# Performance work log

Hardware: AMD Instinct MI355X
Metric: run time of the kernel (lower is better)

The kernel has to match this reference:

```python
import jax, jax.numpy as jnp
import numpy as np

N = 100000
K = 16
C_IN = 64
C_MID = 64   # max(in_channels, out_channels // 2)
C_OUT = 128
EPS = 1e-5


def setup_inputs() -> dict:
    key = jax.random.key(0)
    ks = jax.random.split(key, 4)
    feat = jax.random.normal(ks[0], (N, C_IN), dtype=jnp.float32)
    reference_index = jax.random.randint(ks[1], (N, K), 0, N, dtype=jnp.int64)
    # Kaiming-ish init for the two Linear layers (torch Linear default scale)
    W1 = jax.random.normal(ks[2], (C_IN, C_MID), dtype=jnp.float32) / np.sqrt(C_IN)
    W2 = jax.random.normal(ks[3], (C_MID, C_OUT), dtype=jnp.float32) / np.sqrt(C_MID)
    return {
        "feat": feat,
        "reference_index": reference_index,
        "W1": W1,
        "b1": jnp.zeros((C_MID,), jnp.float32),
        "gamma1": jnp.ones((C_MID,), jnp.float32),
        "beta1": jnp.zeros((C_MID,), jnp.float32),
        "W2": W2,
        "b2": jnp.zeros((C_OUT,), jnp.float32),
        "gamma2": jnp.ones((C_OUT,), jnp.float32),
        "beta2": jnp.zeros((C_OUT,), jnp.float32),
    }


def _bn(x, gamma, beta):
    # BatchNorm1d in training mode: biased batch stats over the row dim.
    mean = jnp.mean(x, axis=0)
    var = jnp.var(x, axis=0)
    return (x - mean) * jax.lax.rsqrt(var + EPS) * gamma + beta


def reference(feat, reference_index, W1, b1, gamma1, beta1, W2, b2, gamma2, beta2):
    # grouping (with_xyz=False): gather neighbor features -> [N, K, C_IN]
    grouped = feat[reference_index]
    x = grouped.reshape(-1, C_IN)                 # [N*K, C_IN]
    h = jax.nn.relu(_bn(x @ W1 + b1, gamma1, beta1))   # [N*K, C_MID]
    h = jax.nn.relu(_bn(h @ W2 + b2, gamma2, beta2))   # [N*K, C_OUT]
    out = h.reshape(N, K, C_OUT).max(axis=1)      # max-pool over neighbors
    return out
```

## Files before the change

kernel.cpp:

```cpp
#include <hip/hip_runtime.h>
#include <hip/hip_bf16.h>

#define N_PTS 100000
#define KNN   16
#define NK    (N_PTS * KNN)
#define CIN   64
#define CMID  64
#define COUT  128

#define HSLC    64
#define SEG_CNT 25000
#define SEG_U32 12500

#define NCOPY 32

#define OFF_PC    0
#define OFF_HB    0
#define OFF_SP1   13000000
#define OFF_SP2   13100000
#define OFF_Z1B   25600000
#define OFF_CNT   38400000
#define OFF_W2BF  38801536
#define OFF_W1BF  38817920

typedef __attribute__((ext_vector_type(8))) short bf16x8;
typedef __attribute__((ext_vector_type(4))) float f32x4;
union U8 { uint4 u; bf16x8 v; unsigned short s[8]; };

__device__ __forceinline__ unsigned short f2bf(float f) {
    unsigned u = __float_as_uint(f);
    unsigned r = (u + 0x7fffu + ((u >> 16) & 1u)) >> 16;
    return (unsigned short)r;
}

__global__ __launch_bounds__(256) void hist_k(const int* __restrict__ idx,
                                              unsigned short* __restrict__ pc,
                                              const float* __restrict__ W2,
                                              unsigned short* __restrict__ w2bf,
                                              const float* __restrict__ W1,
                                              unsigned short* __restrict__ w1bf,
                                              float* __restrict__ sp1,
                                              float* __restrict__ sp2) {
    if (blockIdx.x >= 256) {
        if (blockIdx.x == 256) {
            for (int e = threadIdx.x; e < 8192; e += 256) {
                int j = e & 7, lane = (e >> 3) & 63, kh = (e >> 9) & 1, nt = e >> 10;
                int k = kh * 32 + (lane >> 4) * 8 + j;
                int n = nt * 16 + (lane & 15);
                w2bf[e] = f2bf(W2[k * COUT + n]);
            }
        } else if (blockIdx.x == 257) {
            for (int e = threadIdx.x; e < 4096; e += 256) {
                int j = e & 7, lane = (e >> 3) & 63, kh = (e >> 9) & 1, nt = e >> 10;
                int k = kh * 32 + (lane >> 4) * 8 + j;
                int n = nt * 16 + (lane & 15);
                w1bf[e] = f2bf(W1[k * CMID + n]);
            }
        } else {
            for (int i = threadIdx.x; i < NCOPY * 128; i += 256) sp1[i] = 0.f;
            for (int i = threadIdx.x; i < NCOPY * 256; i += 256) sp2[i] = 0.f;
        }
        return;
    }
    __shared__ unsigned int smem[SEG_U32];
    int seg  = blockIdx.x & 3;
    int slc  = blockIdx.x >> 2;
    int base = seg * SEG_CNT;

    for (int i = threadIdx.x; i < SEG_U32; i += 256) smem[i] = 0;
    __syncthreads();

    const int4* ip = (const int4*)idx;
    const int per = NK / 4 / HSLC;
    int s = slc * per, e = s + per;
    for (int i = s + threadIdx.x; i < e; i += 256) {
        int4 v = ip[i];
        int a;
        a = v.x - base; if ((unsigned)a < (unsigned)SEG_CNT)
            atomicAdd(&smem[a >> 1], 1u << ((a & 1) * 16));
        a = v.y - base; if ((unsigned)a < (unsigned)SEG_CNT)
            atomicAdd(&smem[a >> 1], 1u << ((a & 1) * 16));
        a = v.z - base; if ((unsigned)a < (unsigned)SEG_CNT)
            atomicAdd(&smem[a >> 1], 1u << ((a & 1) * 16));
        a = v.w - base; if ((unsigned)a < (unsigned)SEG_CNT)
            atomicAdd(&smem[a >> 1], 1u << ((a & 1) * 16));
    }
    __syncthreads();

    unsigned int* outp = (unsigned int*)(pc + (size_t)slc * N_PTS) + seg * SEG_U32;
    for (int i = threadIdx.x; i < SEG_U32; i += 256) outp[i] = smem[i];
}

__global__ __launch_bounds__(256) void gemm1_k(const float* __restrict__ feat,
                                               const unsigned short* __restrict__ w1bf,
                                               const float* __restrict__ b1,
                                               const unsigned short* __restrict__ pc,
                                               float* __restrict__ counts,
                                               unsigned short* __restrict__ z1b,
                                               float* __restrict__ sp1) {
    int lane = threadIdx.x & 63, wid = threadIdx.x >> 6;
    int il = lane & 15, quad = lane >> 4;

    bf16x8 wf[4][2];
    const uint4* wp = (const uint4*)w1bf;
    #pragma unroll
    for (int nt = 0; nt < 4; nt++) {
        U8 t0; t0.u = wp[(nt * 2 + 0) * 64 + lane]; wf[nt][0] = t0.v;
        U8 t1; t1.u = wp[(nt * 2 + 1) * 64 + lane]; wf[nt][1] = t1.v;
    }
    float bias[4];
    #pragma unroll
    for (int nt = 0; nt < 4; nt++) bias[nt] = b1[nt * 16 + il];

    float s[4] = {0, 0, 0, 0}, q[4] = {0, 0, 0, 0};

    int wgid = blockIdx.x * 4 + wid;
    for (int tile = wgid; tile < N_PTS / 16; tile += gridDim.x * 4) {
        int m0 = tile * 16;

        const uint4* pcp = (const uint4*)(pc + (size_t)lane * N_PTS + m0);
        uint4 pa = pcp[0], pb = pcp[1];
        #pragma unroll
        for (int m = 1; m < 64; m <<= 1) {
            pa.x += __shfl_xor(pa.x, m, 64);
            pa.y += __shfl_xor(pa.y, m, 64);
            pa.z += __shfl_xor(pa.z, m, 64);
            pa.w += __shfl_xor(pa.w, m, 64);
            pb.x += __shfl_xor(pb.x, m, 64);
            pb.y += __shfl_xor(pb.y, m, 64);
            pb.z += __shfl_xor(pb.z, m, 64);
            pb.w += __shfl_xor(pb.w, m, 64);
        }
        unsigned w0 = (quad == 0) ? pa.x : (quad == 1) ? pa.z : (quad == 2) ? pb.x : pb.z;
        unsigned w1 = (quad == 0) ? pa.y : (quad == 1) ? pa.w : (quad == 2) ? pb.y : pb.w;
        float4 cnt4;
        cnt4.x = (float)(w0 & 0xffffu);
        cnt4.y = (float)(w0 >> 16);
        cnt4.z = (float)(w1 & 0xffffu);
        cnt4.w = (float)(w1 >> 16);
        if (il == 0) ((float4*)(counts + m0))[quad] = cnt4;

        const float* fr = feat + (size_t)(m0 + il) * 64;
        float4 fa = *(const float4*)(fr + quad * 8);
        float4 fb = *(const float4*)(fr + quad * 8 + 4);
        float4 fc = *(const float4*)(fr + 32 + quad * 8);
        float4 fd = *(const float4*)(fr + 32 + quad * 8 + 4);
        U8 ua, ub;
        ua.s[0] = f2bf(fa.x); ua.s[1] = f2bf(fa.y); ua.s[2] = f2bf(fa.z); ua.s[3] = f2bf(fa.w);
        ua.s[4] = f2bf(fb.x); ua.s[5] = f2bf(fb.y); ua.s[6] = f2bf(fb.z); ua.s[7] = f2bf(fb.w);
        ub.s[0] = f2bf(fc.x); ub.s[1] = f2bf(fc.y); ub.s[2] = f2bf(fc.z); ub.s[3] = f2bf(fc.w);
        ub.s[4] = f2bf(fd.x); ub.s[5] = f2bf(fd.y); ub.s[6] = f2bf(fd.z); ub.s[7] = f2bf(fd.w);

        #pragma unroll
        for (int nt = 0; nt < 4; nt++) {
            f32x4 acc = {bias[nt], bias[nt], bias[nt], bias[nt]};
            acc = __builtin_amdgcn_mfma_f32_16x16x32_bf16(ua.v, wf[nt][0], acc, 0, 0, 0);
            acc = __builtin_amdgcn_mfma_f32_16x16x32_bf16(ub.v, wf[nt][1], acc, 0, 0, 0);
            unsigned short* zp = z1b + (size_t)(m0 + quad * 4) * 64 + nt * 16 + il;
            zp[0]   = f2bf(acc[0]);
            zp[64]  = f2bf(acc[1]);
            zp[128] = f2bf(acc[2]);
            zp[192] = f2bf(acc[3]);
            s[nt] += cnt4.x * acc[0] + cnt4.y * acc[1] + cnt4.z * acc[2] + cnt4.w * acc[3];
            q[nt] += cnt4.x * acc[0] * acc[0] + cnt4.y * acc[1] * acc[1]
                   + cnt4.z * acc[2] * acc[2] + cnt4.w * acc[3] * acc[3];
        }
    }
    #pragma unroll
    for (int m = 16; m <= 32; m <<= 1) {
        #pragma unroll
        for (int nt = 0; nt < 4; nt++) {
            s[nt] += __shfl_xor(s[nt], m, 64);
            q[nt] += __shfl_xor(q[nt], m, 64);
        }
    }
    __shared__ float sred[2][4][4][16];
    if (quad == 0) {
        #pragma unroll
        for (int nt = 0; nt < 4; nt++) { sred[0][wid][nt][il] = s[nt]; sred[1][wid][nt][il] = q[nt]; }
    }
    __syncthreads();
    if (threadIdx.x < 128) {
        int which = threadIdx.x >> 6, c = threadIdx.x & 63;
        float t = sred[which][0][c >> 4][c & 15] + sred[which][1][c >> 4][c & 15]
                + sred[which][2][c >> 4][c & 15] + sred[which][3][c >> 4][c & 15];
        atomicAdd(&sp1[(blockIdx.x & (NCOPY - 1)) * 128 + threadIdx.x], t);
    }
}

__device__ __forceinline__ bf16x8 bnrelu(uint4 r, float4 alo, float4 ahi,
                                         float4 blo, float4 bhi) {
    float z0 = __uint_as_float(r.x << 16), z1 = __uint_as_float(r.x & 0xffff0000u);
    float z2 = __uint_as_float(r.y << 16), z3 = __uint_as_float(r.y & 0xffff0000u);
    float z4 = __uint_as_float(r.z << 16), z5 = __uint_as_float(r.z & 0xffff0000u);
    float z6 = __uint_as_float(r.w << 16), z7 = __uint_as_float(r.w & 0xffff0000u);
    U8 o;
    o.s[0] = f2bf(fmaxf(fmaf(alo.x, z0, blo.x), 0.f));
    o.s[1] = f2bf(fmaxf(fmaf(alo.y, z1, blo.y), 0.f));
    o.s[2] = f2bf(fmaxf(fmaf(alo.z, z2, blo.z), 0.f));
    o.s[3] = f2bf(fmaxf(fmaf(alo.w, z3, blo.w), 0.f));
    o.s[4] = f2bf(fmaxf(fmaf(ahi.x, z4, bhi.x), 0.f));
    o.s[5] = f2bf(fmaxf(fmaf(ahi.y, z5, bhi.y), 0.f));
    o.s[6] = f2bf(fmaxf(fmaf(ahi.z, z6, bhi.z), 0.f));
    o.s[7] = f2bf(fmaxf(fmaf(ahi.w, z7, bhi.w), 0.f));
    return o.v;
}

__global__ __launch_bounds__(256) void stats2_k(const unsigned short* __restrict__ z1b,
                                                const unsigned short* __restrict__ w2bf,
                                                const float* __restrict__ sp1,
                                                const float* __restrict__ g1,
                                                const float* __restrict__ be1,
                                                const float* __restrict__ b2,
                                                const float* __restrict__ counts,
                                                unsigned short* __restrict__ hb,
                                                float* __restrict__ sp2) {
    __shared__ float Sl[128];
    __shared__ float Al[64], Bl[64];
    if (threadIdx.x < 128) {
        float t = 0.f;
        #pragma unroll
        for (int k = 0; k < NCOPY; k++) t += sp1[k * 128 + threadIdx.x];
        Sl[threadIdx.x] = t;
    }
    __syncthreads();
    if (threadIdx.x < 64) {
        const float inv = 1.0f / (float)NK;
        float m = Sl[threadIdx.x] * inv;
        float v = Sl[64 + threadIdx.x] * inv - m * m;
        float a = g1[threadIdx.x] * rsqrtf(v + 1e-5f);
        Al[threadIdx.x] = a;
        Bl[threadIdx.x] = be1[threadIdx.x] - m * a;
    }
    __syncthreads();

    int lane = threadIdx.x & 63, wid = threadIdx.x >> 6;
    int il = lane & 15, quad = lane >> 4;

    float4 a0lo = *(const float4*)(Al + quad * 8);
    float4 a0hi = *(const float4*)(Al + quad * 8 + 4);
    float4 b0lo = *(const float4*)(Bl + quad * 8);
    float4 b0hi = *(const float4*)(Bl + quad * 8 + 4);
    float4 a1lo = *(const float4*)(Al + 32 + quad * 8);
    float4 a1hi = *(const float4*)(Al + 32 + quad * 8 + 4);
    float4 b1lo = *(const float4*)(Bl + 32 + quad * 8);
    float4 b1hi = *(const float4*)(Bl + 32 + quad * 8 + 4);

    bf16x8 bfr[8][2];
    const uint4* wp = (const uint4*)w2bf;
    #pragma unroll
    for (int nt = 0; nt < 8; nt++) {
        U8 t0; t0.u = wp[(nt * 2 + 0) * 64 + lane]; bfr[nt][0] = t0.v;
        U8 t1; t1.u = wp[(nt * 2 + 1) * 64 + lane]; bfr[nt][1] = t1.v;
    }
    float bias[8];
    #pragma unroll
    for (int nt = 0; nt < 8; nt++) bias[nt] = b2[nt * 16 + il];

    float s[8], q[8];
    #pragma unroll
    for (int j = 0; j < 8; j++) { s[j] = 0.f; q[j] = 0.f; }

    int wgid = blockIdx.x * 4 + wid;
    for (int tile = wgid; tile < N_PTS / 16; tile += gridDim.x * 4) {
        int m0 = tile * 16;
        const uint4* ar = (const uint4*)(z1b + (size_t)(m0 + il) * 64);
        uint4 ra0 = ar[quad];
        uint4 ra1 = ar[4 + quad];
        bf16x8 af0 = bnrelu(ra0, a0lo, a0hi, b0lo, b0hi);
        bf16x8 af1 = bnrelu(ra1, a1lo, a1hi, b1lo, b1hi);
        U8 o0; o0.v = af0;
        U8 o1; o1.v = af1;
        uint4* hp = (uint4*)(hb + (size_t)(m0 + il) * 64);
        hp[quad]     = o0.u;
        hp[4 + quad] = o1.u;
        float4 cnt4 = *(const float4*)(counts + m0 + quad * 4);
        #pragma unroll
        for (int nt = 0; nt < 8; nt++) {
            f32x4 acc = {bias[nt], bias[nt], bias[nt], bias[nt]};
            acc = __builtin_amdgcn_mfma_f32_16x16x32_bf16(af0, bfr[nt][0], acc, 0, 0, 0);
            acc = __builtin_amdgcn_mfma_f32_16x16x32_bf16(af1, bfr[nt][1], acc, 0, 0, 0);
            s[nt] += cnt4.x * acc[0] + cnt4.y * acc[1] + cnt4.z * acc[2] + cnt4.w * acc[3];
            q[nt] += cnt4.x * acc[0] * acc[0] + cnt4.y * acc[1] * acc[1]
                   + cnt4.z * acc[2] * acc[2] + cnt4.w * acc[3] * acc[3];
        }
    }
    #pragma unroll
    for (int m = 16; m <= 32; m <<= 1) {
        #pragma unroll
        for (int nt = 0; nt < 8; nt++) {
            s[nt] += __shfl_xor(s[nt], m, 64);
            q[nt] += __shfl_xor(q[nt], m, 64);
        }
    }
    __shared__ float sred[2][4][8][16];
    if (quad == 0) {
        #pragma unroll
        for (int nt = 0; nt < 8; nt++) { sred[0][wid][nt][il] = s[nt]; sred[1][wid][nt][il] = q[nt]; }
    }
    __syncthreads();
    {
        int which = threadIdx.x >> 7, c = threadIdx.x & 127;
        float t = sred[which][0][c >> 4][c & 15] + sred[which][1][c >> 4][c & 15]
                + sred[which][2][c >> 4][c & 15] + sred[which][3][c >> 4][c & 15];
        atomicAdd(&sp2[(blockIdx.x & (NCOPY - 1)) * 256 + threadIdx.x], t);
    }
}

__global__ __launch_bounds__(256) void fused_k(const unsigned short* __restrict__ hb,
                                               const unsigned short* __restrict__ w2bf,
                                               const int* __restrict__ idx,
                                               const float* __restrict__ b2,
                                               const float* __restrict__ sp2,
                                               const float* __restrict__ g2,
                                               const float* __restrict__ be2,
                                               float* __restrict__ out) {
    __shared__ float S2l[256];
    __shared__ float A2s[128], B2f[128];
    __shared__ uint4 wlds[1024];

    {
        float t = 0.f;
        #pragma unroll
        for (int k = 0; k < NCOPY; k++) t += sp2[k * 256 + threadIdx.x];
        S2l[threadIdx.x] = t;
    }
    __syncthreads();
    const float inv = 1.0f / (float)NK;
    if (threadIdx.x < 128) {
        int c = threadIdx.x;
        float m = S2l[c] * inv;
        float v = S2l[128 + c] * inv - m * m;
        float a = g2[c] * rsqrtf(v + 1e-5f);
        A2s[c] = a;
        B2f[c] = fmaf(a, b2[c], be2[c] - m * a);
    }
    __syncthreads();

    for (int i = threadIdx.x; i < 1024; i += 256) {
        uint4 w = ((const uint4*)w2bf)[i];
        int n_ = ((i >> 7) << 4) + (i & 15);
        if (A2s[n_] < 0.f) {
            w.x ^= 0x80008000u; w.y ^= 0x80008000u;
            w.z ^= 0x80008000u; w.w ^= 0x80008000u;
        }
        wlds[i] = w;
    }
    __syncthreads();

    int lane = threadIdx.x & 63, wid = threadIdx.x >> 6;
    int il = lane & 15, quad = lane >> 4;

    bf16x8 bfr[8][2];
    #pragma unroll
    for (int nt = 0; nt < 8; nt++) {
        U8 t0; t0.u = wlds[(nt * 2 + 0) * 64 + lane]; bfr[nt][0] = t0.v;
        U8 t1; t1.u = wlds[(nt * 2 + 1) * 64 + lane]; bfr[nt][1] = t1.v;
    }
    float a2c[8], b2c[8];
    #pragma unroll
    for (int nt = 0; nt < 8; nt++) {
        a2c[nt] = fabsf(A2s[nt * 16 + il]);
        b2c[nt] = B2f[nt * 16 + il];
    }

    const int stride = gridDim.x * 4;
    int n  = blockIdx.x * 4 + wid;
    int n1 = n + stride;

    uint4 r0c = {0, 0, 0, 0}, r1c = {0, 0, 0, 0};
    if (n < N_PTS) {
        int j0 = idx[(size_t)n * KNN + il];
        const uint4* zr = (const uint4*)(hb + (size_t)j0 * 64);
        r0c = zr[quad];
        r1c = zr[4 + quad];
    }
    int j1 = (n1 < N_PTS) ? idx[(size_t)n1 * KNN + il] : 0;

    while (n < N_PTS) {
        uint4 r0n = {0, 0, 0, 0}, r1n = {0, 0, 0, 0};
        int n2 = n1 + stride;
        if (n1 < N_PTS) {
            const uint4* zr = (const uint4*)(hb + (size_t)j1 * 64);
            r0n = zr[quad];
            r1n = zr[4 + quad];
        }
        int j2 = (n2 < N_PTS) ? idx[(size_t)n2 * KNN + il] : 0;

        U8 ua, ub; ua.u = r0c; ub.u = r1c;
        float w0 = 0.f, w1 = 0.f;
        #pragma unroll
        for (int nt = 0; nt < 8; nt++) {
            f32x4 acc = {0.f, 0.f, 0.f, 0.f};
            acc = __builtin_amdgcn_mfma_f32_16x16x32_bf16(ua.v, bfr[nt][0], acc, 0, 0, 0);
            acc = __builtin_amdgcn_mfma_f32_16x16x32_bf16(ub.v, bfr[nt][1], acc, 0, 0, 0);
            float t = fmaxf(fmaxf(acc[0], acc[1]), fmaxf(acc[2], acc[3]));
            t = fmaxf(t, __shfl_xor(t, 16, 64));
            t = fmaxf(t, __shfl_xor(t, 32, 64));
            float v = fmaxf(fmaf(a2c[nt], t, b2c[nt]), 0.f);
            if (nt == quad)     w0 = v;
            if (nt == quad + 4) w1 = v;
        }
        float* op = out + (size_t)n * COUT;
        __builtin_nontemporal_store(w0, op + quad * 16 + il);
        __builtin_nontemporal_store(w1, op + 64 + quad * 16 + il);

        n = n1; n1 = n2; j1 = j2;
        r0c = r0n; r1c = r1n;
    }
}

extern "C" void kernel_launch(void* const* d_in, const int* in_sizes, int n_in,
                              void* d_out, int out_size, void* d_ws, size_t ws_size,
                              hipStream_t stream) {
    const float* feat = (const float*)d_in[0];
    const int*   idx  = (const int*)d_in[1];
    const float* W1   = (const float*)d_in[2];
    const float* b1   = (const float*)d_in[3];
    const float* g1   = (const float*)d_in[4];
    const float* be1  = (const float*)d_in[5];
    const float* W2   = (const float*)d_in[6];
    const float* b2   = (const float*)d_in[7];
    const float* g2   = (const float*)d_in[8];
    const float* be2  = (const float*)d_in[9];
    float* out = (float*)d_out;

    char* ws = (char*)d_ws;
    unsigned short* pc  = (unsigned short*)(ws + OFF_PC);
    unsigned short* hb  = (unsigned short*)(ws + OFF_HB);
    float* sp1 = (float*)(ws + OFF_SP1);
    float* sp2 = (float*)(ws + OFF_SP2);
    unsigned short* z1b = (unsigned short*)(ws + OFF_Z1B);
    float* counts = (float*)(ws + OFF_CNT);
    unsigned short* w2bf = (unsigned short*)(ws + OFF_W2BF);
    unsigned short* w1bf = (unsigned short*)(ws + OFF_W1BF);

    hist_k<<<259, 256, 0, stream>>>(idx, pc, W2, w2bf, W1, w1bf, sp1, sp2);
    gemm1_k<<<512, 256, 0, stream>>>(feat, w1bf, b1, pc, counts, z1b, sp1);
    stats2_k<<<512, 256, 0, stream>>>(z1b, w2bf, sp1, g1, be1, b2, counts, hb, sp2);
    fused_k<<<2048, 256, 0, stream>>>(hb, w2bf, idx, b2, sp2, g2, be2, out);
}
```

Before: 180.0 us.

## Use 32x32x16 MFMA in fused kernel, processing two points per wave

The final fused gather-GEMM-maxpool kernel switches from 16x16x32 bf16 MFMA on one point per wave to 32x32x16 MFMA covering two points (32 neighbor rows) per wave. A second W2 bf16 layout matching the 32x32 operand format is built in the prep kernel. This halves the loop trip count, cuts the cross-lane shuffles needed for the max reduction, and makes each lane store one contiguous output value per column tile. In exchange it needs more accumulator registers and an extra weight layout in the workspace.

```diff
diff --git a/kernel.cpp b/kernel.cpp
--- a/kernel.cpp
+++ b/kernel.cpp
@@ -14,17 +14,19 @@
 
 #define NCOPY 32
 
-#define OFF_PC    0
-#define OFF_HB    0
-#define OFF_SP1   13000000
-#define OFF_SP2   13100000
-#define OFF_Z1B   25600000
-#define OFF_CNT   38400000
-#define OFF_W2BF  38801536
-#define OFF_W1BF  38817920
+#define OFF_PC     0
+#define OFF_HB     0
+#define OFF_SP1    13000000
+#define OFF_SP2    13100000
+#define OFF_W2BF32 13200000
+#define OFF_Z1B    25600000
+#define OFF_CNT    38400000
+#define OFF_W2BF   38801536
+#define OFF_W1BF   38817920
 
 typedef __attribute__((ext_vector_type(8))) short bf16x8;
 typedef __attribute__((ext_vector_type(4))) float f32x4;
+typedef __attribute__((ext_vector_type(16))) float f32x16;
 union U8 { uint4 u; bf16x8 v; unsigned short s[8]; };
 
 __device__ __forceinline__ unsigned short f2bf(float f) {
@@ -37,6 +39,7 @@
                                               unsigned short* __restrict__ pc,
                                               const float* __restrict__ W2,
                                               unsigned short* __restrict__ w2bf,
+                                              unsigned short* __restrict__ w2bf32,
                                               const float* __restrict__ W1,
                                               unsigned short* __restrict__ w1bf,
                                               float* __restrict__ sp1,
@@ -48,6 +51,13 @@
                 int k = kh * 32 + (lane >> 4) * 8 + j;
                 int n = nt * 16 + (lane & 15);
                 w2bf[e] = f2bf(W2[k * COUT + n]);
+            }
+            for (int e = threadIdx.x; e < 8192; e += 256) {
+                int j = e & 7, lane = (e >> 3) & 63, f = e >> 9;
+                int kc = f & 3, nt2 = f >> 2;
+                int k = kc * 16 + (lane >> 5) * 8 + j;
+                int n = nt2 * 32 + (lane & 31);
+                w2bf32[e] = f2bf(W2[k * COUT + n]);
             }
         } else if (blockIdx.x == 257) {
             for (int e = threadIdx.x; e < 4096; e += 256) {
@@ -308,7 +318,7 @@
 }
 
 __global__ __launch_bounds__(256) void fused_k(const unsigned short* __restrict__ hb,
-                                               const unsigned short* __restrict__ w2bf,
+                                               const unsigned short* __restrict__ w2bf32,
                                                const int* __restrict__ idx,
                                                const float* __restrict__ b2,
                                                const float* __restrict__ sp2,
@@ -338,9 +348,9 @@
     __syncthreads();
 
     for (int i = threadIdx.x; i < 1024; i += 256) {
-        uint4 w = ((const uint4*)w2bf)[i];
-        int n_ = ((i >> 7) << 4) + (i & 15);
-        if (A2s[n_] < 0.f) {
+        uint4 w = ((const uint4*)w2bf32)[i];
+        int c = ((i >> 8) << 5) + (i & 31);
+        if (A2s[c] < 0.f) {
             w.x ^= 0x80008000u; w.y ^= 0x80008000u;
             w.z ^= 0x80008000u; w.w ^= 0x80008000u;
         }
@@ -349,64 +359,73 @@
     __syncthreads();
 
     int lane = threadIdx.x & 63, wid = threadIdx.x >> 6;
-    int il = lane & 15, quad = lane >> 4;
-
-    bf16x8 bfr[8][2];
-    #pragma unroll
-    for (int nt = 0; nt < 8; nt++) {
-        U8 t0; t0.u = wlds[(nt * 2 + 0) * 64 + lane]; bfr[nt][0] = t0.v;
-        U8 t1; t1.u = wlds[(nt * 2 + 1) * 64 + lane]; bfr[nt][1] = t1.v;
-    }
-    float a2c[8], b2c[8];
-    #pragma unroll
-    for (int nt = 0; nt < 8; nt++) {
-        a2c[nt] = fabsf(A2s[nt * 16 + il]);
-        b2c[nt] = B2f[nt * 16 + il];
-    }
-
+    int r32 = lane & 31;
+    int hi  = lane >> 5;
+    int pl  = (lane >> 4) & 1;
+    int nb  = lane & 15;
+
+    bf16x8 bfr[4][4];
+    #pragma unroll
+    for (int nt2 = 0; nt2 < 4; nt2++) {
+        #pragma unroll
+        for (int kc = 0; kc < 4; kc++) {
+            U8 t; t.u = wlds[(nt2 * 4 + kc) * 64 + lane];
+            bfr[nt2][kc] = t.v;
+        }
+    }
+    float a2c[4], b2c[4];
+    #pragma unroll
+    for (int nt2 = 0; nt2 < 4; nt2++) {
+        a2c[nt2] = fabsf(A2s[nt2 * 32 + r32]);
+        b2c[nt2] = B2f[nt2 * 32 + r32];
+    }
+
+    const int NPAIRS = N_PTS / 2;
     const int stride = gridDim.x * 4;
-    int n  = blockIdx.x * 4 + wid;
-    int n1 = n + stride;
-
-    uint4 r0c = {0, 0, 0, 0}, r1c = {0, 0, 0, 0};
-    if (n < N_PTS) {
-        int j0 = idx[(size_t)n * KNN + il];
-        const uint4* zr = (const uint4*)(hb + (size_t)j0 * 64);
-        r0c = zr[quad];
-        r1c = zr[4 + quad];
-    }
-    int j1 = (n1 < N_PTS) ? idx[(size_t)n1 * KNN + il] : 0;
-
-    while (n < N_PTS) {
-        uint4 r0n = {0, 0, 0, 0}, r1n = {0, 0, 0, 0};
-        int n2 = n1 + stride;
-        if (n1 < N_PTS) {
-            const uint4* zr = (const uint4*)(hb + (size_t)j1 * 64);
-            r0n = zr[quad];
-            r1n = zr[4 + quad];
-        }
-        int j2 = (n2 < N_PTS) ? idx[(size_t)n2 * KNN + il] : 0;
-
-        U8 ua, ub; ua.u = r0c; ub.u = r1c;
-        float w0 = 0.f, w1 = 0.f;
-        #pragma unroll
-        for (int nt = 0; nt < 8; nt++) {
-            f32x4 acc = {0.f, 0.f, 0.f, 0.f};
-            acc = __builtin_amdgcn_mfma_f32_16x16x32_bf16(ua.v, bfr[nt][0], acc, 0, 0, 0);
-            acc = __builtin_amdgcn_mfma_f32_16x16x32_bf16(ub.v, bfr[nt][1], acc, 0, 0, 0);
-            float t = fmaxf(fmaxf(acc[0], acc[1]), fmaxf(acc[2], acc[3]));
-            t = fmaxf(t, __shfl_xor(t, 16, 64));
-            t = fmaxf(t, __shfl_xor(t, 32, 64));
-            float v = fmaxf(fmaf(a2c[nt], t, b2c[nt]), 0.f);
-            if (nt == quad)     w0 = v;
-            if (nt == quad + 4) w1 = v;
-        }
-        float* op = out + (size_t)n * COUT;
-        __builtin_nontemporal_store(w0, op + quad * 16 + il);
-        __builtin_nontemporal_store(w1, op + 64 + quad * 16 + il);
-
-        n = n1; n1 = n2; j1 = j2;
-        r0c = r0n; r1c = r1n;
+    int pair = blockIdx.x * 4 + wid;
+    int p1 = pair + stride;
+
+    uint4 rc0 = {0,0,0,0}, rc1 = {0,0,0,0}, rc2 = {0,0,0,0}, rc3 = {0,0,0,0};
+    if (pair < NPAIRS) {
+        int j0 = idx[(size_t)(pair * 2 + pl) * KNN + nb];
+        const uint4* zr = (const uint4*)hb + (size_t)j0 * 8;
+        rc0 = zr[0 + hi]; rc1 = zr[2 + hi]; rc2 = zr[4 + hi]; rc3 = zr[6 + hi];
+    }
+    int j1 = (p1 < NPAIRS) ? idx[(size_t)(p1 * 2 + pl) * KNN + nb] : 0;
+
+    while (pair < NPAIRS) {
+        uint4 rn0 = {0,0,0,0}, rn1 = {0,0,0,0}, rn2 = {0,0,0,0}, rn3 = {0,0,0,0};
+        int p2 = p1 + stride;
+        if (p1 < NPAIRS) {
+            const uint4* zr = (const uint4*)hb + (size_t)j1 * 8;
+            rn0 = zr[0 + hi]; rn1 = zr[2 + hi]; rn2 = zr[4 + hi]; rn3 = zr[6 + hi];
+        }
+        int j2 = (p2 < NPAIRS) ? idx[(size_t)(p2 * 2 + pl) * KNN + nb] : 0;
+
+        U8 a0, a1, a2, a3;
+        a0.u = rc0; a1.u = rc1; a2.u = rc2; a3.u = rc3;
+        #pragma unroll
+        for (int nt2 = 0; nt2 < 4; nt2++) {
+            f32x16 acc = {0.f,0.f,0.f,0.f,0.f,0.f,0.f,0.f,0.f,0.f,0.f,0.f,0.f,0.f,0.f,0.f};
+            acc = __builtin_amdgcn_mfma_f32_32x32x16_bf16(a0.v, bfr[nt2][0], acc, 0, 0, 0);
+            acc = __builtin_amdgcn_mfma_f32_32x32x16_bf16(a1.v, bfr[nt2][1], acc, 0, 0, 0);
+            acc = __builtin_amdgcn_mfma_f32_32x32x16_bf16(a2.v, bfr[nt2][2], acc, 0, 0, 0);
+            acc = __builtin_amdgcn_mfma_f32_32x32x16_bf16(a3.v, bfr[nt2][3], acc, 0, 0, 0);
+            float mxA = fmaxf(fmaxf(fmaxf(acc[0], acc[1]), fmaxf(acc[2], acc[3])),
+                              fmaxf(fmaxf(acc[4], acc[5]), fmaxf(acc[6], acc[7])));
+            float mxB = fmaxf(fmaxf(fmaxf(acc[8], acc[9]), fmaxf(acc[10], acc[11])),
+                              fmaxf(fmaxf(acc[12], acc[13]), fmaxf(acc[14], acc[15])));
+            mxA = fmaxf(mxA, __shfl_xor(mxA, 32, 64));
+            mxB = fmaxf(mxB, __shfl_xor(mxB, 32, 64));
+            float vA = fmaxf(fmaf(a2c[nt2], mxA, b2c[nt2]), 0.f);
+            float vB = fmaxf(fmaf(a2c[nt2], mxB, b2c[nt2]), 0.f);
+            float vv = hi ? vB : vA;
+            int np = pair * 2 + hi;
+            __builtin_nontemporal_store(vv, out + (size_t)np * COUT + nt2 * 32 + r32);
+        }
+
+        pair = p1; p1 = p2; j1 = j2;
+        rc0 = rn0; rc1 = rn1; rc2 = rn2; rc3 = rn3;
     }
 }
 
@@ -430,13 +449,14 @@
     unsigned short* hb  = (unsigned short*)(ws + OFF_HB);
     float* sp1 = (float*)(ws + OFF_SP1);
     float* sp2 = (float*)(ws + OFF_SP2);
+    unsigned short* w2bf32 = (unsigned short*)(ws + OFF_W2BF32);
     unsigned short* z1b = (unsigned short*)(ws + OFF_Z1B);
     float* counts = (float*)(ws + OFF_CNT);
     unsigned short* w2bf = (unsigned short*)(ws + OFF_W2BF);
     unsigned short* w1bf = (unsigned short*)(ws + OFF_W1BF);
 
-    hist_k<<<259, 256, 0, stream>>>(idx, pc, W2, w2bf, W1, w1bf, sp1, sp2);
+    hist_k<<<259, 256, 0, stream>>>(idx, pc, W2, w2bf, w2bf32, W1, w1bf, sp1, sp2);
     gemm1_k<<<512, 256, 0, stream>>>(feat, w1bf, b1, pc, counts, z1b, sp1);
     stats2_k<<<512, 256, 0, stream>>>(z1b, w2bf, sp1, g1, be1, b2, counts, hb, sp2);
-    fused_k<<<2048, 256, 0, stream>>>(hb, w2bf, idx, b2, sp2, g2, be2, out);
-}
+    fused_k<<<2048, 256, 0, stream>>>(hb, w2bf32, idx, b2, sp2, g2, be2, out);
+}
```

After: 176.8 us. Within noise of the previous version (-1.8%).
